# Performance work log

Measured on AMD Instinct MI355X. Metric: run time of the kernel, lower is better.

Reference implementation:

```python
import jax, jax.numpy as jnp
import numpy as np

# Dimensions: T total prefill tokens, S ragged segments (one adapter each),
# M target modules sharing this linear, r LoRA rank.
T, D_IN, D_OUT, R, M, S = 8192, 4096, 4096, 16, 2, 8


def setup_inputs() -> dict:
    key = jax.random.key(0)
    ks = jax.random.split(key, 6)
    x = jax.random.normal(ks[0], (T, D_IN), dtype=jnp.float32)
    W = jax.random.normal(ks[1], (D_OUT, D_IN), dtype=jnp.float32) * 0.02
    b = jax.random.normal(ks[2], (D_OUT,), dtype=jnp.float32) * 0.02
    # lora_A[m, s] = A.T of adapter s for target module m: [D_IN, R]
    lora_A = jax.random.normal(ks[3], (M, S, D_IN, R), dtype=jnp.float32) * 0.02
    # lora_B[m, s] = B.T: [R, D_OUT]
    lora_B = jax.random.normal(ks[4], (M, S, R, D_OUT), dtype=jnp.float32) * 0.02
    cu = jnp.sort(jax.random.randint(ks[5], (S + 1,), 0, T + 1, dtype=jnp.int32))
    cu = cu.at[0].set(0).at[-1].set(T)  # segment boundaries cover [0, T)
    return {"x": x, "W": W, "b": b, "lora_A": lora_A, "lora_B": lora_B,
            "cu_seqlen": cu}


def reference(x, W, b, lora_A, lora_B, cu_seqlen):
    # Base linear: out = x @ W.T + b
    out = x @ W.T + b
    tok = jnp.arange(x.shape[0])
    n_seg = lora_A.shape[1]
    # SGMV-style ragged LoRA: tokens in segment s use adapter s for every
    # target module m; contributions from all modules add into `out`.
    # Masking (instead of dynamic slicing) keeps shapes static / jit-friendly
    # and is exact: masked-out tokens contribute zero.
    for s in range(n_seg):
        mask = ((tok >= cu_seqlen[s]) & (tok < cu_seqlen[s + 1]))
        xm = x * mask.astype(x.dtype)[:, None]            # [T, D_IN], zero outside segment
        u = jnp.einsum('td,mdr->tmr', xm, lora_A[:, s])    # [T, M, R] low-rank down-proj
        out = out + jnp.einsum('tmr,mrD->tD', u, lora_B[:, s])  # up-proj, sum over modules
    return out
```

## Files before the change

kernel.cpp:

```cpp
#include <hip/hip_runtime.h>
#include <hip/hip_bf16.h>

#define T_TOK 8192
#define DIN   4096
#define DOUT  4096
#define RANK  16
#define NMOD  2
#define NSEG  8

typedef __attribute__((ext_vector_type(8))) short bf16x8;
typedef __attribute__((ext_vector_type(8))) unsigned short u16x8;
typedef __attribute__((ext_vector_type(4))) float f32x4;

__device__ inline unsigned short f2bf(float f) {
    union { float f; unsigned u; } v; v.f = f;
    unsigned r = v.u + 0x7FFFu + ((v.u >> 16) & 1u);
    return (unsigned short)(r >> 16);
}

__device__ inline void gload_lds16(const void* g, void* l) {
    __builtin_amdgcn_global_load_lds(
        (const __attribute__((address_space(1))) void*)g,
        (__attribute__((address_space(3))) void*)l, 16, 0, 0);
}

__global__ void cast2_bf16_kernel(const float* __restrict__ sa,
                                  unsigned short* __restrict__ da, int n8a,
                                  const float* __restrict__ sb,
                                  unsigned short* __restrict__ db, int n8b) {
    int i = blockIdx.x * blockDim.x + threadIdx.x;
    const float* s;
    unsigned short* d;
    size_t j;
    if (i < n8a) { s = sa; d = da; j = (size_t)i; }
    else if (i < n8a + n8b) { s = sb; d = db; j = (size_t)(i - n8a); }
    else return;
    const float4* s4 = (const float4*)s;
    float4 a = s4[2 * j];
    float4 b = s4[2 * j + 1];
    u16x8 o;
    o[0] = f2bf(a.x); o[1] = f2bf(a.y); o[2] = f2bf(a.z); o[3] = f2bf(a.w);
    o[4] = f2bf(b.x); o[5] = f2bf(b.y); o[6] = f2bf(b.z); o[7] = f2bf(b.w);
    *(u16x8*)(d + 8 * j) = o;
}

__global__ void prep_A_kernel(const float* __restrict__ A,
                              unsigned short* __restrict__ At) {
    int idx = blockIdx.x * 256 + threadIdx.x;
    int d   = idx & (DIN - 1);
    int smr = idx >> 12;
    int s   = smr >> 5, mr = smr & 31;
    int m   = mr >> 4,  r  = mr & 15;
    float v = A[(((size_t)(m * NSEG + s) * DIN) + d) * RANK + r];
    At[idx] = f2bf(v);
}

__global__ void prep_B_kernel(const float* __restrict__ B,
                              unsigned short* __restrict__ Bt) {
    int o  = blockIdx.x * 256 + threadIdx.x;
    int s  = o >> 12;
    int oc = o & (DOUT - 1);
    unsigned short tmp[32];
    for (int m = 0; m < NMOD; ++m)
        for (int r = 0; r < RANK; ++r)
            tmp[m * 16 + r] =
                f2bf(B[(((size_t)(m * NSEG + s) * RANK) + r) * DOUT + oc]);
    for (int k = 0; k < 4; ++k) {
        u16x8 v;
        for (int j = 0; j < 8; ++j) v[j] = tmp[k * 8 + j];
        *(u16x8*)(Bt + (size_t)o * 32 + k * 8) = v;
    }
}

__global__ __launch_bounds__(64) void u_gemm_kernel(
    const unsigned short* __restrict__ xb, const unsigned short* __restrict__ At,
    const int* __restrict__ cu, float* __restrict__ Pu) {
    int tile = blockIdx.x;
    int ky   = blockIdx.y;
    int lane = threadIdx.x;
    int l15  = lane & 15, lk = lane >> 4;
    int t0   = tile * 32;
    f32x4 acc[2][2] = {};
    bf16x8 zero = {};
    for (int s = 0; s < NSEG; ++s) {
        int lo = cu[s], hi = cu[s + 1];
        if (hi <= t0 || lo >= t0 + 32) continue;
        const unsigned short* atb = At + (size_t)(s * 32) * DIN;
        for (int kt = 0; kt < 32; ++kt) {
            int k0 = ky * 1024 + kt * 32 + lk * 8;
            bf16x8 a[2], b[2];
            for (int mi = 0; mi < 2; ++mi) {
                int row = t0 + mi * 16 + l15;
                bf16x8 av = *(const bf16x8*)(xb + (size_t)row * DIN + k0);
                a[mi] = (row >= lo && row < hi) ? av : zero;
            }
            for (int ni = 0; ni < 2; ++ni) {
                int mr = ni * 16 + l15;
                b[ni] = *(const bf16x8*)(atb + (size_t)mr * DIN + k0);
            }
            for (int mi = 0; mi < 2; ++mi)
                for (int ni = 0; ni < 2; ++ni)
                    acc[mi][ni] = __builtin_amdgcn_mfma_f32_16x16x32_bf16(
                        a[mi], b[ni], acc[mi][ni], 0, 0, 0);
        }
    }
    for (int mi = 0; mi < 2; ++mi)
        for (int ni = 0; ni < 2; ++ni)
            for (int j = 0; j < 4; ++j) {
                int t  = t0 + mi * 16 + lk * 4 + j;
                int mr = ni * 16 + l15;
                Pu[((size_t)ky * T_TOK + t) * 32 + mr] = acc[mi][ni][j];
            }
}

__global__ void reduce_u_kernel(const float* __restrict__ Pu,
                                unsigned short* __restrict__ ub) {
    int idx = blockIdx.x * 256 + threadIdx.x;
    const size_t STRIDE = (size_t)T_TOK * 32;
    float s = Pu[idx] + Pu[idx + STRIDE] + Pu[idx + 2 * STRIDE] + Pu[idx + 3 * STRIDE];
    ub[idx] = f2bf(s);
}


__device__ __forceinline__ bf16x8 fragA(const char* mat, int row, int lk) {
    int rb = (row << 6) + ((lk ^ ((row >> 1) & 3)) << 4);
    return *(const bf16x8*)(mat + rb);
}

#define STAGE_R(GB_, LD_, TB_, K0_)                                           \
  { int tb = (TB_);                                                            \
    int lrow = tb >> 6;                                                        \
    int cb = (tb & 63) ^ (((lrow >> 1) & 3) << 4);                             \
    gload_lds16((GB_) + (size_t)lrow * DIN + (K0_) + (cb >> 1), (LD_) + tb); }

#define BODY(T_, S_, STG_, VM_, BAR_)                                          \
  {                                                                            \
    const char* cA = lds + (S_) * 32768;                                       \
    const char* cB = cA + 16384;                                               \
    char* sA = lds + (1 - (S_)) * 32768;                                       \
    char* sB = sA + 16384;                                                     \
    const int k0n = ((T_) + 1) * 32;                                           \
    bf16x8 af[8], bf[4];                                                       \
    for (int n = 0; n < 4; ++n) bf[n] = fragA(cB, wcol + n*16 + l15, lk);      \
    for (int m = 0; m < 8; ++m) af[m] = fragA(cA, wrow + m*16 + l15, lk);      \
    if (STG_) {                                                                \
        STAGE_R(xrow, sA, tid*16, k0n);                                        \
        STAGE_R(xrow, sA, 8192 + tid*16, k0n);                                 \
        STAGE_R(wrow_g, sB, tid*16, k0n);                                      \
        STAGE_R(wrow_g, sB, 8192 + tid*16, k0n);                               \
    }                                                                          \
    __builtin_amdgcn_s_setprio(1);                                             \
    for (int m = 0; m < 8; ++m)                                                \
        for (int n = 0; n < 4; ++n)                                            \
            acc[m][n] = __builtin_amdgcn_mfma_f32_16x16x32_bf16(               \
                af[m], bf[n], acc[m][n], 0, 0, 0);                             \
    __builtin_amdgcn_s_setprio(0);                                             \
    if ((VM_) >= 0) asm volatile("s_waitcnt vmcnt(0)" ::: "memory");           \
    if (BAR_) __builtin_amdgcn_s_barrier();                                    \
  }

__global__ __launch_bounds__(512, 2) void main_gemm_kernel(
    const unsigned short* __restrict__ xb, const unsigned short* __restrict__ wb,
    const unsigned short* __restrict__ ub, const unsigned short* __restrict__ bt,
    const float* __restrict__ bias, const int* __restrict__ cu,
    float* __restrict__ out) {
    __shared__ __attribute__((aligned(1024))) char lds[65536];
    int tid  = threadIdx.x;
    int w    = tid >> 6, lane = tid & 63;
    int l15  = lane & 15, lk = lane >> 4;
    int wrow = (w >> 2) * 128;
    int wcol = (w & 3) * 64;
    int xcd   = blockIdx.x & 7;
    int local = blockIdx.x >> 3;
    int colp  = xcd * 2 + (local >> 5);
    int rowp  = local & 31;
    int row0 = rowp * 256, col0 = colp * 256;

    const unsigned short* xrow   = xb + (size_t)row0 * DIN;
    const unsigned short* wrow_g = wb + (size_t)col0 * DIN;

    f32x4 acc[8][4] = {};

    STAGE_R(xrow, lds, tid*16, 0);
    STAGE_R(xrow, lds, 8192 + tid*16, 0);
    STAGE_R(wrow_g, lds + 16384, tid*16, 0);
    STAGE_R(wrow_g, lds + 16384, 8192 + tid*16, 0);
    asm volatile("s_waitcnt vmcnt(0)" ::: "memory");
    __builtin_amdgcn_s_barrier();

    #pragma unroll 1
    for (int t = 0; t < 126; t += 2) {
        BODY(t,     0, 1, 0, 1);
        BODY(t + 1, 1, 1, 0, 1);
    }
    BODY(126, 0, 1, 0, 1);
    BODY(127, 1, 0, -1, 0);

    bf16x8 zero = {};
    for (int s = 0; s < NSEG; ++s) {
        int lo = cu[s], hi = cu[s + 1];
        if (hi <= row0 || lo >= row0 + 256) continue;
        bf16x8 au[8], bu[4];
        for (int m = 0; m < 8; ++m) {
            int row = row0 + wrow + m * 16 + l15;
            bf16x8 v = *(const bf16x8*)(ub + (size_t)row * 32 + lk * 8);
            au[m] = (row >= lo && row < hi) ? v : zero;
        }
        for (int n = 0; n < 4; ++n) {
            int col = col0 + wcol + n * 16 + l15;
            bu[n] = *(const bf16x8*)(bt + ((size_t)s * DOUT + col) * 32 + lk * 8);
        }
        for (int m = 0; m < 8; ++m)
            for (int n = 0; n < 4; ++n)
                acc[m][n] = __builtin_amdgcn_mfma_f32_16x16x32_bf16(
                    au[m], bu[n], acc[m][n], 0, 0, 0);
    }

    float bv[4];
    for (int n = 0; n < 4; ++n) bv[n] = bias[col0 + wcol + n * 16 + l15];
    for (int m = 0; m < 8; ++m) {
        int rbase = row0 + wrow + m * 16 + lk * 4;
        for (int n = 0; n < 4; ++n) {
            int col = col0 + wcol + n * 16 + l15;
            for (int jj = 0; jj < 4; ++jj)
                out[(size_t)(rbase + jj) * DOUT + col] = acc[m][n][jj] + bv[n];
        }
    }
}

extern "C" void kernel_launch(void* const* d_in, const int* in_sizes, int n_in,
                              void* d_out, int out_size, void* d_ws, size_t ws_size,
                              hipStream_t stream) {
    const float* x  = (const float*)d_in[0];
    const float* W  = (const float*)d_in[1];
    const float* b  = (const float*)d_in[2];
    const float* lA = (const float*)d_in[3];
    const float* lB = (const float*)d_in[4];
    const int*   cu = (const int*)d_in[5];
    float* out = (float*)d_out;

    char* ws = (char*)d_ws;
    unsigned short* xb = (unsigned short*)(ws);
    unsigned short* wb = (unsigned short*)(ws + 67108864);
    unsigned short* At = (unsigned short*)(ws + 100663296);
    unsigned short* Bt = (unsigned short*)(ws + 102760448);
    float*          Pu = (float*)(ws + 104857600);
    unsigned short* ub = (unsigned short*)(ws + 109051904);

    const int n8x = T_TOK * DIN / 8, n8w = DOUT * DIN / 8;
    cast2_bf16_kernel<<<(n8x + n8w) / 256, 256, 0, stream>>>(x, xb, n8x, W, wb, n8w);
    prep_A_kernel<<<(NSEG * 32 * DIN) / 256, 256, 0, stream>>>(lA, At);
    prep_B_kernel<<<(NSEG * DOUT) / 256, 256, 0, stream>>>(lB, Bt);
    dim3 ug(T_TOK / 32, 4);
    u_gemm_kernel<<<ug, 64, 0, stream>>>(xb, At, cu, Pu);
    reduce_u_kernel<<<(T_TOK * 32) / 256, 256, 0, stream>>>(Pu, ub);
    dim3 mg(32 * 16);
    main_gemm_kernel<<<mg, 512, 0, stream>>>(xb, wb, ub, Bt, b, cu, out);
}
```

Baseline: 348.0 us.

## Replace barrier double-buffering with triple-buffered LDS and per-wave counter sync

Moves the main GEMM K-loop from a two-stage LDS ring synchronized by workgroup barriers to a three-stage ring, prefetching two tiles ahead. Waves now coordinate through LDS ready/done counters polled with atomics instead of barriers, so each wave loads and consumes tiles at its own pace. The block-to-tile mapping is also re-swizzled across XCDs. The cost is 96KB of LDS per block, which may cut occupancy below the two blocks per CU that launch_bounds requests, plus spin-polling overhead and the risk of subtle synchronization bugs.

```diff
diff --git a/kernel.cpp b/kernel.cpp
--- a/kernel.cpp
+++ b/kernel.cpp
@@ -127,74 +127,85 @@
     return *(const bf16x8*)(mat + rb);
 }
 
-#define STAGE_R(GB_, LD_, TB_, K0_)                                           \
-  { int tb = (TB_);                                                            \
-    int lrow = tb >> 6;                                                        \
-    int cb = (tb & 63) ^ (((lrow >> 1) & 3) << 4);                             \
-    gload_lds16((GB_) + (size_t)lrow * DIN + (K0_) + (cb >> 1), (LD_) + tb); }
-
-#define BODY(T_, S_, STG_, VM_, BAR_)                                          \
-  {                                                                            \
-    const char* cA = lds + (S_) * 32768;                                       \
-    const char* cB = cA + 16384;                                               \
-    char* sA = lds + (1 - (S_)) * 32768;                                       \
-    char* sB = sA + 16384;                                                     \
-    const int k0n = ((T_) + 1) * 32;                                           \
-    bf16x8 af[8], bf[4];                                                       \
-    for (int n = 0; n < 4; ++n) bf[n] = fragA(cB, wcol + n*16 + l15, lk);      \
-    for (int m = 0; m < 8; ++m) af[m] = fragA(cA, wrow + m*16 + l15, lk);      \
-    if (STG_) {                                                                \
-        STAGE_R(xrow, sA, tid*16, k0n);                                        \
-        STAGE_R(xrow, sA, 8192 + tid*16, k0n);                                 \
-        STAGE_R(wrow_g, sB, tid*16, k0n);                                      \
-        STAGE_R(wrow_g, sB, 8192 + tid*16, k0n);                               \
-    }                                                                          \
-    __builtin_amdgcn_s_setprio(1);                                             \
-    for (int m = 0; m < 8; ++m)                                                \
-        for (int n = 0; n < 4; ++n)                                            \
-            acc[m][n] = __builtin_amdgcn_mfma_f32_16x16x32_bf16(               \
-                af[m], bf[n], acc[m][n], 0, 0, 0);                             \
-    __builtin_amdgcn_s_setprio(0);                                             \
-    if ((VM_) >= 0) asm volatile("s_waitcnt vmcnt(0)" ::: "memory");           \
-    if (BAR_) __builtin_amdgcn_s_barrier();                                    \
-  }
+__device__ __forceinline__ void poll_ge(unsigned int* p, unsigned int tgt) {
+    while (__hip_atomic_load(p, __ATOMIC_RELAXED, __HIP_MEMORY_SCOPE_WORKGROUP) < tgt)
+        __builtin_amdgcn_s_sleep(1);
+}
+
+#define STAGE_W(T_, S_)                                                        \
+  { char* sA_ = lds + (S_) * 32768;                                            \
+    char* sB_ = sA_ + 16384;                                                   \
+    int k0_ = (T_) * 32;                                                       \
+    for (int i_ = 0; i_ < 2; ++i_) {                                           \
+        int tb_ = w * 2048 + i_ * 1024 + lane * 16;                            \
+        int lrow_ = tb_ >> 6;                                                  \
+        int cb_ = (tb_ & 63) ^ (((lrow_ >> 1) & 3) << 4);                      \
+        gload_lds16(xrow + (size_t)lrow_ * DIN + k0_ + (cb_ >> 1), sA_ + tb_); \
+        gload_lds16(wrow_g + (size_t)lrow_ * DIN + k0_ + (cb_ >> 1), sB_ + tb_);\
+    } }
 
 __global__ __launch_bounds__(512, 2) void main_gemm_kernel(
     const unsigned short* __restrict__ xb, const unsigned short* __restrict__ wb,
     const unsigned short* __restrict__ ub, const unsigned short* __restrict__ bt,
     const float* __restrict__ bias, const int* __restrict__ cu,
     float* __restrict__ out) {
-    __shared__ __attribute__((aligned(1024))) char lds[65536];
+    __shared__ __attribute__((aligned(1024))) char lds[98304];
+    __shared__ unsigned int ready_cnt[3];
+    __shared__ unsigned int done_cnt[3];
     int tid  = threadIdx.x;
     int w    = tid >> 6, lane = tid & 63;
     int l15  = lane & 15, lk = lane >> 4;
     int wrow = (w >> 2) * 128;
     int wcol = (w & 3) * 64;
-    int xcd   = blockIdx.x & 7;
-    int local = blockIdx.x >> 3;
-    int colp  = xcd * 2 + (local >> 5);
-    int rowp  = local & 31;
-    int row0 = rowp * 256, col0 = colp * 256;
+    int swz  = (blockIdx.x & 7) * 64 + (blockIdx.x >> 3);
+    int row0 = (swz >> 4) * 256;
+    int col0 = (swz & 15) * 256;
 
     const unsigned short* xrow   = xb + (size_t)row0 * DIN;
     const unsigned short* wrow_g = wb + (size_t)col0 * DIN;
 
     f32x4 acc[8][4] = {};
 
-    STAGE_R(xrow, lds, tid*16, 0);
-    STAGE_R(xrow, lds, 8192 + tid*16, 0);
-    STAGE_R(wrow_g, lds + 16384, tid*16, 0);
-    STAGE_R(wrow_g, lds + 16384, 8192 + tid*16, 0);
+    if (tid == 0) {
+        ready_cnt[0] = 8; ready_cnt[1] = 8; ready_cnt[2] = 0;
+        done_cnt[0] = 0; done_cnt[1] = 0; done_cnt[2] = 0;
+    }
+    STAGE_W(0, 0);
+    STAGE_W(1, 1);
     asm volatile("s_waitcnt vmcnt(0)" ::: "memory");
-    __builtin_amdgcn_s_barrier();
+    __syncthreads();
 
     #pragma unroll 1
-    for (int t = 0; t < 126; t += 2) {
-        BODY(t,     0, 1, 0, 1);
-        BODY(t + 1, 1, 1, 0, 1);
-    }
-    BODY(126, 0, 1, 0, 1);
-    BODY(127, 1, 0, -1, 0);
+    for (int t = 0; t < 128; ++t) {
+        int s = t % 3;
+        if (t >= 1 && t + 2 <= 127) {
+            poll_ge(&done_cnt[(t + 2) % 3], 8u * (unsigned)((t - 1) / 3 + 1));
+            __builtin_amdgcn_sched_barrier(0);
+        }
+        if (t + 2 <= 127) STAGE_W(t + 2, (t + 2) % 3);
+        if (t >= 1 && t <= 126) {
+            if (t + 2 <= 127) asm volatile("s_waitcnt vmcnt(4)" ::: "memory");
+            else              asm volatile("s_waitcnt vmcnt(0)" ::: "memory");
+            __builtin_amdgcn_sched_barrier(0);
+            if (lane == 0) atomicAdd(&ready_cnt[(t + 1) % 3], 1u);
+            __builtin_amdgcn_sched_barrier(0);
+        }
+        poll_ge(&ready_cnt[s], 8u * (unsigned)(t / 3 + 1));
+        __builtin_amdgcn_sched_barrier(0);
+        const char* cA = lds + s * 32768;
+        const char* cB = cA + 16384;
+        bf16x8 af[8], bf[4];
+        for (int n = 0; n < 4; ++n) bf[n] = fragA(cB, wcol + n * 16 + l15, lk);
+        for (int m = 0; m < 8; ++m) af[m] = fragA(cA, wrow + m * 16 + l15, lk);
+        __builtin_amdgcn_s_setprio(1);
+        for (int m = 0; m < 8; ++m)
+            for (int n = 0; n < 4; ++n)
+                acc[m][n] = __builtin_amdgcn_mfma_f32_16x16x32_bf16(
+                    af[m], bf[n], acc[m][n], 0, 0, 0);
+        __builtin_amdgcn_s_setprio(0);
+        __builtin_amdgcn_sched_barrier(0);
+        if (lane == 0) atomicAdd(&done_cnt[s], 1u);
+    }
 
     bf16x8 zero = {};
     for (int s = 0; s < NSEG; ++s) {
```

Measured after the change: 433.3 us. 1.25x slower.
